# Performance work log

Measured on AMD Instinct MI355X. Metric: run time of the kernel, lower is better.

The kernel has to match this reference:

```python
import jax, jax.numpy as jnp
import numpy as np

B, S, E, H, L, NQ, FFN, V, C = 16, 2048, 256, 4, 2, 8, 512, 50257, 2
DK = E // H  # wires per attention head


def _pos_encoding(seq_len, dim):
    pos = jnp.arange(seq_len, dtype=jnp.float32)[:, None]
    div = jnp.exp(jnp.arange(0, dim, 2, dtype=jnp.float32) * (-np.log(10000.0) / dim))
    pe = jnp.zeros((seq_len, dim), dtype=jnp.float32)
    pe = pe.at[:, 0::2].set(jnp.sin(pos * div))
    pe = pe.at[:, 1::2].set(jnp.cos(pos * div))
    return pe


def _layernorm(x, g, b, eps=1e-5):
    m = x.mean(-1, keepdims=True)
    v = ((x - m) ** 2).mean(-1, keepdims=True)
    return (x - m) / jnp.sqrt(v + eps) * g + b


def setup_inputs() -> dict:
    key = jax.random.key(0)
    ks = jax.random.split(key, 9)
    f = lambda k, shape, s: jax.random.normal(k, shape, dtype=jnp.float32) * s
    return {
        "tokens": jax.random.randint(ks[0], (B, S), 0, V),
        "embed": f(ks[1], (V, E), 0.02),
        "attn_theta": f(ks[2], (L, DK), 1.0),
        "combine_w": f(ks[3], (L, E, E), 0.05),
        "combine_b": jnp.zeros((L, E), jnp.float32),
        "ffn_theta": f(ks[4], (L, NQ), 1.0),
        "lin1_w": f(ks[5], (L, NQ, FFN), 0.1),
        "lin1_b": jnp.zeros((L, FFN), jnp.float32),
        "lin2_w": f(ks[6], (L, FFN, E), 0.05),
        "lin2_b": jnp.zeros((L, E), jnp.float32),
        "ln1_g": jnp.ones((L, E), jnp.float32),
        "ln1_b": jnp.zeros((L, E), jnp.float32),
        "ln2_g": jnp.ones((L, E), jnp.float32),
        "ln2_b": jnp.zeros((L, E), jnp.float32),
        "cls_w": f(ks[7], (E, C), 0.05),
        "cls_b": jnp.zeros((C,), jnp.float32),
    }


def reference(tokens, embed, attn_theta, combine_w, combine_b, ffn_theta,
              lin1_w, lin1_b, lin2_w, lin2_b, ln1_g, ln1_b, ln2_g, ln2_b,
              cls_w, cls_b):
    # token embedding + sinusoidal positional encoding
    x = embed[tokens] + _pos_encoding(S, E)[None]  # [B,S,E]
    for l in range(L):
        # QuantumAttention: per-head RX-encode(x) then trainable RX(theta),
        # PauliZ expectation => cos(x + theta); same theta shared across heads,
        # head split/merge preserves feature layout => tile theta over heads.
        theta = jnp.tile(attn_theta[l], H)  # [E]
        attn = jnp.einsum('bse,ef->bsf', jnp.cos(x + theta), combine_w[l]) + combine_b[l]
        x = _layernorm(x + attn, ln1_g[l], ln1_b[l])
        # FeedForwardQuantum: RX-encode first NQ features, trainable RY(theta),
        # PauliZ expectation => cos(x) * cos(theta)
        q = jnp.cos(x[..., :NQ]) * jnp.cos(ffn_theta[l])  # [B,S,NQ]
        h = jax.nn.relu(jnp.einsum('bsn,nf->bsf', q, lin1_w[l]) + lin1_b[l])
        ffn = jnp.einsum('bsf,fe->bse', h, lin2_w[l]) + lin2_b[l]
        x = _layernorm(x + ffn, ln2_g[l], ln2_b[l])
    pooled = x.mean(axis=1)  # [B,E]
    return pooled @ cls_w + cls_b  # [B,C] logits
```

## Files before the change

### kernel.cpp

```cpp
#include <hip/hip_runtime.h>
#include <cstdint>
#include <cstddef>

#define SEQ   2048
#define EDIM  256
#define FFND  512
#define NBATCH 16
#define XLD   264

typedef unsigned short u16;
typedef __attribute__((ext_vector_type(8))) __bf16 bf16x8;
typedef __attribute__((ext_vector_type(4))) float f32x4;

__device__ __forceinline__ float bf2f(u16 u) {
  union { unsigned int w; float f; } v; v.w = ((unsigned int)u) << 16; return v.f;
}
__device__ __forceinline__ u16 f2bf(float f) {
  union { float f; unsigned int w; } v; v.f = f;
  unsigned int r = v.w + 0x7fffu + ((v.w >> 16) & 1u);
  return (u16)(r >> 16);
}
__device__ __forceinline__ float fast_cos(float x) {
  float r = x * 0.15915494309189535f;
  r = r - floorf(r);
  return __builtin_amdgcn_cosf(r);
}
__device__ __forceinline__ void unpack8(bf16x8 v, float* o) {
  const u16* p = (const u16*)&v;
  #pragma unroll
  for (int j = 0; j < 8; ++j) o[j] = bf2f(p[j]);
}

__global__ void sniff_kernel(const void* embed, int* flag) {
  int t = threadIdx.x;
  const u16* p = (const u16*)embed;
  int c = 0;
  #pragma unroll
  for (int j = 0; j < 8; ++j) {
    u16 v = p[t * 8 + j];
    int e = (v >> 7) & 0xff;
    c += (e > 128) ? 1 : 0;
  }
  #pragma unroll
  for (int d = 1; d < 64; d <<= 1) c += __shfl_xor(c, d);
  if (t == 0) *flag = (c > 64) ? 1 : 0;
}

struct CanonArgs { const void* p[14]; };

__global__ void canon_kernel(CanonArgs a, const int* __restrict__ flag, u16* __restrict__ dst) {
  const int off[15] = {0, 128, 131200, 131712, 131728, 139920, 140944, 403088,
                       403600, 404112, 404624, 405136, 405648, 406160, 406162};
  int i = blockIdx.x * 256 + threadIdx.x;
  if (i >= 406162) return;
  int isf32 = *flag;
  int s = 0;
  #pragma unroll
  for (int k = 0; k < 13; ++k) s += (i >= off[k + 1]) ? 1 : 0;
  int j = i - off[s];
  u16 v = isf32 ? f2bf(((const float*)a.p[s])[j]) : ((const u16*)a.p[s])[j];
  dst[i] = v;
}

__global__ void prep_kernel(const u16* __restrict__ cw, const u16* __restrict__ l2,
                            u16* __restrict__ cwT, u16* __restrict__ l2T) {
  int id = blockIdx.x * 256 + threadIdx.x;
  if (id < 2 * 256 * 256) {
    int l = id >> 16, rem = id & 65535;
    int kc = rem >> 11, n = (rem >> 3) & 255, kj = rem & 7;
    cwT[id] = cw[l * 65536 + (kc * 8 + kj) * 256 + n];
  } else {
    int j = id - 131072;
    if (j < 2 * 512 * 256) {
      int l = j >> 17, rem = j & 131071;
      int kc = rem >> 11, n = (rem >> 3) & 255, kj = rem & 7;
      l2T[j] = l2[l * 131072 + (kc * 8 + kj) * 256 + n];
    }
  }
}

__launch_bounds__(256, 2)
__global__ void mega_kernel(const int* __restrict__ tokens, const void* __restrict__ embed,
                            const int* __restrict__ flag, const u16* __restrict__ canon,
                            const u16* __restrict__ cwT, const u16* __restrict__ l2T,
                            float* __restrict__ pooled) {
  __shared__ u16 xt[64 * XLD];
  __shared__ union {
    struct { u16 Bt[256 * 64]; u16 At[64 * 64]; u16 qs[64 * 8]; } k;
    struct { float2 sstat[64][5]; float2 sms[64]; } ln;
  } sh;
  __shared__ u16 thL[64];

  const int tid = threadIdx.x;
  const int wave = tid >> 6, lane = tid & 63;
  const int fr = lane & 15, fq = lane >> 4;
  const int m0 = blockIdx.x * 64;
  const int isf32 = *flag;

  int cols[4];
  #pragma unroll
  for (int ni = 0; ni < 4; ++ni) cols[ni] = wave * 64 + ni * 16 + fr;

  {
    const float c0 = 9.210340371976184f / 128.f;
    const float inv2pi = 0.15915494309189535f;
    #pragma unroll
    for (int it = 0; it < 8; ++it) {
      int c = it * 256 + tid;
      int r = c >> 5, e8 = c & 31;
      int tok = tokens[m0 + r];
      float ev[8];
      if (isf32) {
        const float* ep = (const float*)embed + (size_t)tok * EDIM + e8 * 8;
        float4 a = *(const float4*)ep, b = *(const float4*)(ep + 4);
        ev[0]=a.x; ev[1]=a.y; ev[2]=a.z; ev[3]=a.w; ev[4]=b.x; ev[5]=b.y; ev[6]=b.z; ev[7]=b.w;
      } else {
        const u16* ep = (const u16*)embed + (size_t)tok * EDIM + e8 * 8;
        uint4 v = *(const uint4*)ep;
        unpack8(*(const bf16x8*)&v, ev);
      }
      int s = (m0 + r) & (SEQ - 1);
      u16 o[8];
      #pragma unroll
      for (int j = 0; j < 8; ++j) {
        int e = e8 * 8 + j, i = e >> 1;
        float rev = (float)s * (__expf(-(float)i * c0) * inv2pi);
        rev = rev - floorf(rev);
        float pe = (e & 1) ? __builtin_amdgcn_cosf(rev) : __builtin_amdgcn_sinf(rev);
        o[j] = f2bf(ev[j] + pe);
      }
      *(uint4*)(xt + r * XLD + e8 * 8) = *(const uint4*)o;
    }
  }
  __syncthreads();

  f32x4 acc[4][4];

  auto mfma_step = [&]() {
    const bf16x8* Av = (const bf16x8*)sh.k.At;
    const bf16x8* Bv = (const bf16x8*)sh.k.Bt;
    #pragma unroll
    for (int ks = 0; ks < 2; ++ks) {
      const int kc = ks * 4 + fq;
      bf16x8 af[4], bfv[4];
      #pragma unroll
      for (int mi = 0; mi < 4; ++mi) af[mi] = Av[kc * 64 + ((mi * 16 + fr) ^ kc)];
      #pragma unroll
      for (int ni = 0; ni < 4; ++ni) bfv[ni] = Bv[kc * 256 + cols[ni]];
      #pragma unroll
      for (int mi = 0; mi < 4; ++mi)
        #pragma unroll
        for (int ni = 0; ni < 4; ++ni)
          acc[mi][ni] = __builtin_amdgcn_mfma_f32_16x16x32_bf16(af[mi], bfv[ni], acc[mi][ni], 0, 0, 0);
    }
  };

  auto epilogue = [&](const u16* bias, const u16* gamma, const u16* beta) {
    float bcol[4];
    #pragma unroll
    for (int ni = 0; ni < 4; ++ni) bcol[ni] = bf2f(bias[cols[ni]]);
    #pragma unroll
    for (int mi = 0; mi < 4; ++mi)
      #pragma unroll
      for (int rg = 0; rg < 4; ++rg) {
        int lrow = mi * 16 + fq * 4 + rg;
        #pragma unroll
        for (int ni = 0; ni < 4; ++ni)
          acc[mi][ni][rg] += bf2f(xt[lrow * XLD + cols[ni]]) + bcol[ni];
      }
    float sr[4][4], sq[4][4];
    #pragma unroll
    for (int mi = 0; mi < 4; ++mi)
      #pragma unroll
      for (int rg = 0; rg < 4; ++rg) {
        float a = 0.f, b = 0.f;
        #pragma unroll
        for (int ni = 0; ni < 4; ++ni) { float t2 = acc[mi][ni][rg]; a += t2; b += t2 * t2; }
        sr[mi][rg] = a; sq[mi][rg] = b;
      }
    #pragma unroll
    for (int d = 1; d < 16; d <<= 1)
      #pragma unroll
      for (int mi = 0; mi < 4; ++mi)
        #pragma unroll
        for (int rg = 0; rg < 4; ++rg) {
          sr[mi][rg] += __shfl_xor(sr[mi][rg], d);
          sq[mi][rg] += __shfl_xor(sq[mi][rg], d);
        }
    if (fr == 0) {
      #pragma unroll
      for (int mi = 0; mi < 4; ++mi)
        #pragma unroll
        for (int rg = 0; rg < 4; ++rg)
          sh.ln.sstat[mi * 16 + fq * 4 + rg][wave] = float2{sr[mi][rg], sq[mi][rg]};
    }
    __syncthreads();
    if (tid < 64) {
      float s = 0.f, s2 = 0.f;
      #pragma unroll
      for (int w = 0; w < 4; ++w) { float2 p = sh.ln.sstat[tid][w]; s += p.x; s2 += p.y; }
      float mean = s * (1.f / 256.f);
      float var = fmaxf(s2 * (1.f / 256.f) - mean * mean, 0.f);
      sh.ln.sms[tid] = float2{mean, rsqrtf(var + 1e-5f)};
    }
    __syncthreads();
    float gcol[4], btc[4];
    #pragma unroll
    for (int ni = 0; ni < 4; ++ni) { gcol[ni] = bf2f(gamma[cols[ni]]); btc[ni] = bf2f(beta[cols[ni]]); }
    #pragma unroll
    for (int mi = 0; mi < 4; ++mi)
      #pragma unroll
      for (int rg = 0; rg < 4; ++rg) {
        int lrow = mi * 16 + fq * 4 + rg;
        float2 ms = sh.ln.sms[lrow];
        #pragma unroll
        for (int ni = 0; ni < 4; ++ni) {
          float o = (acc[mi][ni][rg] - ms.x) * ms.y * gcol[ni] + btc[ni];
          xt[lrow * XLD + cols[ni]] = f2bf(o);
        }
      }
    __syncthreads();
  };

  for (int l = 0; l < 2; ++l) {
    if (tid < 8) ((uint4*)thL)[tid] = ((const uint4*)(canon + l * 64))[tid];
    __syncthreads();
    #pragma unroll
    for (int i = 0; i < 4; ++i)
      #pragma unroll
      for (int j = 0; j < 4; ++j) acc[i][j] = {0.f, 0.f, 0.f, 0.f};
    {
      const u16* Bbase = cwT + l * 65536;
      for (int k0 = 0; k0 < 256; k0 += 64) {
        const u16* bsrc = Bbase + (k0 >> 3) * 2048;
        #pragma unroll
        for (int it = 0; it < 8; ++it) {
          int c = tid + it * 256;
          __builtin_amdgcn_global_load_lds(
              (const __attribute__((address_space(1))) void*)(bsrc + (size_t)c * 8),
              (__attribute__((address_space(3))) void*)(sh.k.Bt + c * 8), 16, 0, 0);
        }
        #pragma unroll
        for (int it = 0; it < 2; ++it) {
          int c = it * 256 + tid;
          int f8 = c >> 6, r = c & 63;
          uint4 g = *(const uint4*)(xt + r * XLD + k0 + f8 * 8);
          u16* gp = (u16*)&g;
          #pragma unroll
          for (int j = 0; j < 8; ++j)
            gp[j] = f2bf(fast_cos(bf2f(gp[j]) + bf2f(thL[f8 * 8 + j])));
          ((uint4*)sh.k.At)[f8 * 64 + (r ^ f8)] = g;
        }
        __syncthreads();
        mfma_step();
        __syncthreads();
      }
    }
    epilogue(canon + 131200 + l * 256, canon + 403600 + l * 256, canon + 404112 + l * 256);

    #pragma unroll
    for (int rep = 0; rep < 2; ++rep) {
      int idx = tid + rep * 256;
      int r = idx >> 3, n = idx & 7;
      float cth = fast_cos(bf2f(canon[131712 + l * 8 + n]));
      sh.k.qs[r * 8 + n] = f2bf(fast_cos(bf2f(xt[r * XLD + n])) * cth);
    }
    __syncthreads();

    #pragma unroll
    for (int i = 0; i < 4; ++i)
      #pragma unroll
      for (int j = 0; j < 4; ++j) acc[i][j] = {0.f, 0.f, 0.f, 0.f};
    {
      const u16* B2 = l2T + l * 131072;
      const u16* w1 = canon + 131728 + l * 4096;
      const u16* b1 = canon + 139920 + l * 512;
      for (int k0 = 0; k0 < 512; k0 += 64) {
        const u16* bsrc = B2 + (k0 >> 3) * 2048;
        #pragma unroll
        for (int it = 0; it < 8; ++it) {
          int c = tid + it * 256;
          __builtin_amdgcn_global_load_lds(
              (const __attribute__((address_space(1))) void*)(bsrc + (size_t)c * 8),
              (__attribute__((address_space(3))) void*)(sh.k.Bt + c * 8), 16, 0, 0);
        }
        #pragma unroll
        for (int it = 0; it < 2; ++it) {
          int c = it * 256 + tid;
          int kc = c >> 6, r = c & 63;
          int cc = (k0 >> 3) + kc;
          float qf[8], hv[8];
          unpack8(((const bf16x8*)sh.k.qs)[r], qf);
          { uint4 bv = *(const uint4*)(b1 + cc * 8); unpack8(*(const bf16x8*)&bv, hv); }
          #pragma unroll
          for (int n = 0; n < 8; ++n) {
            uint4 wv = *(const uint4*)(w1 + n * 512 + cc * 8);
            float wf[8];
            unpack8(*(const bf16x8*)&wv, wf);
            #pragma unroll
            for (int j = 0; j < 8; ++j) hv[j] += qf[n] * wf[j];
          }
          uint4 g; u16* gp = (u16*)&g;
          #pragma unroll
          for (int j = 0; j < 8; ++j) gp[j] = f2bf(fmaxf(hv[j], 0.f));
          ((uint4*)sh.k.At)[kc * 64 + (r ^ kc)] = g;
        }
        __syncthreads();
        mfma_step();
        __syncthreads();
      }
    }
    epilogue(canon + 403088 + l * 256, canon + 404624 + l * 256, canon + 405136 + l * 256);
  }

  {
    float s = 0.f;
    #pragma unroll 8
    for (int r = 0; r < 64; ++r) s += bf2f(xt[r * XLD + tid]);
    atomicAdd(&pooled[(m0 >> 11) * EDIM + tid], s);
  }
}

__global__ void logits_kernel(const float* __restrict__ pooled, const u16* __restrict__ clsw,
                              const u16* __restrict__ clsb, const int* __restrict__ flag,
                              void* __restrict__ out) {
  int t = threadIdx.x;
  int b = t >> 4, sub = t & 15;
  float a0 = 0.f, a1 = 0.f;
  #pragma unroll
  for (int j = 0; j < 16; ++j) {
    int e = sub * 16 + j;
    float p = pooled[b * 256 + e];
    a0 += p * bf2f(clsw[e * 2 + 0]);
    a1 += p * bf2f(clsw[e * 2 + 1]);
  }
  #pragma unroll
  for (int d = 1; d < 16; d <<= 1) {
    a0 += __shfl_xor(a0, d);
    a1 += __shfl_xor(a1, d);
  }
  if (sub == 0) {
    float o0 = a0 * (1.f / 2048.f) + bf2f(clsb[0]);
    float o1 = a1 * (1.f / 2048.f) + bf2f(clsb[1]);
    if (*flag) {
      ((float*)out)[b * 2 + 0] = o0; ((float*)out)[b * 2 + 1] = o1;
    } else {
      ((u16*)out)[b * 2 + 0] = f2bf(o0); ((u16*)out)[b * 2 + 1] = f2bf(o1);
    }
  }
}

extern "C" void kernel_launch(void* const* d_in, const int* in_sizes, int n_in,
                              void* d_out, int out_size, void* d_ws, size_t ws_size,
                              hipStream_t stream) {
  const int* tokens = (const int*)d_in[0];

  char* ws = (char*)d_ws;
  u16*   canon  = (u16*)(ws + 0);
  u16*   cwT    = (u16*)(ws + 1048576);
  u16*   l2T    = (u16*)(ws + 1310720);
  float* pooled = (float*)(ws + 1835008);
  int*   flag   = (int*)(ws + 1851392);

  sniff_kernel<<<1, 64, 0, stream>>>(d_in[1], flag);

  CanonArgs ca;
  for (int i = 0; i < 14; ++i) ca.p[i] = d_in[i + 2];
  canon_kernel<<<1587, 256, 0, stream>>>(ca, flag, canon);

  prep_kernel<<<1536, 256, 0, stream>>>(canon + 128, canon + 140944, cwT, l2T);

  hipMemsetAsync(pooled, 0, NBATCH * EDIM * sizeof(float), stream);

  mega_kernel<<<512, 256, 0, stream>>>(tokens, d_in[1], flag, canon, cwT, l2T, pooled);

  logits_kernel<<<1, 256, 0, stream>>>(pooled, canon + 405648, canon + 406160, flag, d_out);
}
```

Measured before the change: 217.9 us.

## Move FFN lin1 to MFMA, precompute PE divisors, shrink canon copy

The scalar FMA computation of the FFN first layer (q @ lin1_w + b, ReLU) is replaced with MFMA instructions. Weights are held in registers and results are written straight into the swizzled A tile, and the first lin2 B tile is prefetched earlier. Positional-encoding divisors are computed once into a small table, so the per-element exp disappears. Biases are folded into the accumulator init, and packed bf16 conversion uses v_cvt_pk_bf16_f32. The canon/prep kernels now convert the large weights directly from the inputs, so the full copy of combine_w and lin2_w is no longer made twice. The zero-padded MFMA for the K=8 product wastes most lanes, and the inline asm conversion changes rounding details slightly.

```diff
diff --git a/kernel.cpp b/kernel.cpp
--- a/kernel.cpp
+++ b/kernel.cpp
@@ -4,7 +4,6 @@
 
 #define SEQ   2048
 #define EDIM  256
-#define FFND  512
 #define NBATCH 16
 #define XLD   264
 
@@ -20,6 +19,11 @@
   unsigned int r = v.w + 0x7fffu + ((v.w >> 16) & 1u);
   return (u16)(r >> 16);
 }
+__device__ __forceinline__ unsigned int pk2(float lo, float hi) {
+  unsigned int d;
+  asm("v_cvt_pk_bf16_f32 %0, %1, %2" : "=v"(d) : "v"(lo), "v"(hi));
+  return d;
+}
 __device__ __forceinline__ float fast_cos(float x) {
   float r = x * 0.15915494309189535f;
   r = r - floorf(r);
@@ -46,35 +50,50 @@
   if (t == 0) *flag = (c > 64) ? 1 : 0;
 }
 
-struct CanonArgs { const void* p[14]; };
-
-__global__ void canon_kernel(CanonArgs a, const int* __restrict__ flag, u16* __restrict__ dst) {
-  const int off[15] = {0, 128, 131200, 131712, 131728, 139920, 140944, 403088,
-                       403600, 404112, 404624, 405136, 405648, 406160, 406162};
+struct CanonArgs { const void* p[11]; };
+
+__global__ void canon_kernel(CanonArgs a, const int* __restrict__ flag,
+                             u16* __restrict__ dst, float* __restrict__ divt) {
+  const int off[12] = {0, 128, 640, 656, 1680, 2192, 2704, 3216, 3728, 4240, 4752, 4754};
   int i = blockIdx.x * 256 + threadIdx.x;
-  if (i >= 406162) return;
+  if (i < 128) {
+    const float c0 = 9.210340371976184f / 128.f;
+    const float inv2pi = 0.15915494309189535f;
+    divt[i] = __expf(-(float)i * c0) * inv2pi;
+  }
+  if (i >= 4754) return;
   int isf32 = *flag;
   int s = 0;
   #pragma unroll
-  for (int k = 0; k < 13; ++k) s += (i >= off[k + 1]) ? 1 : 0;
+  for (int k = 0; k < 10; ++k) s += (i >= off[k + 1]) ? 1 : 0;
   int j = i - off[s];
-  u16 v = isf32 ? f2bf(((const float*)a.p[s])[j]) : ((const u16*)a.p[s])[j];
-  dst[i] = v;
-}
-
-__global__ void prep_kernel(const u16* __restrict__ cw, const u16* __restrict__ l2,
-                            u16* __restrict__ cwT, u16* __restrict__ l2T) {
+  dst[i] = isf32 ? f2bf(((const float*)a.p[s])[j]) : ((const u16*)a.p[s])[j];
+}
+
+__global__ void prep_kernel(const void* __restrict__ cw, const void* __restrict__ w1,
+                            const void* __restrict__ l2, const int* __restrict__ flag,
+                            u16* __restrict__ cwT, u16* __restrict__ l2T,
+                            u16* __restrict__ w1T) {
   int id = blockIdx.x * 256 + threadIdx.x;
-  if (id < 2 * 256 * 256) {
+  int isf32 = *flag;
+  if (id < 131072) {
     int l = id >> 16, rem = id & 65535;
     int kc = rem >> 11, n = (rem >> 3) & 255, kj = rem & 7;
-    cwT[id] = cw[l * 65536 + (kc * 8 + kj) * 256 + n];
+    int idx = l * 65536 + (kc * 8 + kj) * 256 + n;
+    cwT[id] = isf32 ? f2bf(((const float*)cw)[idx]) : ((const u16*)cw)[idx];
+  } else if (id < 131072 + 262144) {
+    int j = id - 131072;
+    int l = j >> 17, rem = j & 131071;
+    int kc = rem >> 11, n = (rem >> 3) & 255, kj = rem & 7;
+    int idx = l * 131072 + (kc * 8 + kj) * 256 + n;
+    l2T[j] = isf32 ? f2bf(((const float*)l2)[idx]) : ((const u16*)l2)[idx];
   } else {
-    int j = id - 131072;
-    if (j < 2 * 512 * 256) {
-      int l = j >> 17, rem = j & 131071;
-      int kc = rem >> 11, n = (rem >> 3) & 255, kj = rem & 7;
-      l2T[j] = l2[l * 131072 + (kc * 8 + kj) * 256 + n];
+    int j = id - (131072 + 262144);
+    if (j < 2 * 512 * 8) {
+      int l = j >> 12, rem = j & 4095;
+      int c = rem >> 3, jj = rem & 7;
+      int idx = l * 4096 + jj * 512 + c;
+      w1T[j] = isf32 ? f2bf(((const float*)w1)[idx]) : ((const u16*)w1)[idx];
     }
   }
 }
@@ -83,6 +102,7 @@
 __global__ void mega_kernel(const int* __restrict__ tokens, const void* __restrict__ embed,
                             const int* __restrict__ flag, const u16* __restrict__ canon,
                             const u16* __restrict__ cwT, const u16* __restrict__ l2T,
+                            const u16* __restrict__ w1T, const float* __restrict__ divt,
                             float* __restrict__ pooled) {
   __shared__ u16 xt[64 * XLD];
   __shared__ union {
@@ -102,8 +122,6 @@
   for (int ni = 0; ni < 4; ++ni) cols[ni] = wave * 64 + ni * 16 + fr;
 
   {
-    const float c0 = 9.210340371976184f / 128.f;
-    const float inv2pi = 0.15915494309189535f;
     #pragma unroll
     for (int it = 0; it < 8; ++it) {
       int c = it * 256 + tid;
@@ -119,17 +137,18 @@
         uint4 v = *(const uint4*)ep;
         unpack8(*(const bf16x8*)&v, ev);
       }
-      int s = (m0 + r) & (SEQ - 1);
-      u16 o[8];
-      #pragma unroll
-      for (int j = 0; j < 8; ++j) {
-        int e = e8 * 8 + j, i = e >> 1;
-        float rev = (float)s * (__expf(-(float)i * c0) * inv2pi);
-        rev = rev - floorf(rev);
-        float pe = (e & 1) ? __builtin_amdgcn_cosf(rev) : __builtin_amdgcn_sinf(rev);
-        o[j] = f2bf(ev[j] + pe);
-      }
-      *(uint4*)(xt + r * XLD + e8 * 8) = *(const uint4*)o;
+      float sf = (float)((m0 + r) & (SEQ - 1));
+      float4 dv = *(const float4*)(divt + e8 * 4);
+      float r0 = sf * dv.x; r0 -= floorf(r0);
+      float r1 = sf * dv.y; r1 -= floorf(r1);
+      float r2 = sf * dv.z; r2 -= floorf(r2);
+      float r3 = sf * dv.w; r3 -= floorf(r3);
+      uint4 o;
+      o.x = pk2(ev[0] + __builtin_amdgcn_sinf(r0), ev[1] + __builtin_amdgcn_cosf(r0));
+      o.y = pk2(ev[2] + __builtin_amdgcn_sinf(r1), ev[3] + __builtin_amdgcn_cosf(r1));
+      o.z = pk2(ev[4] + __builtin_amdgcn_sinf(r2), ev[5] + __builtin_amdgcn_cosf(r2));
+      o.w = pk2(ev[6] + __builtin_amdgcn_sinf(r3), ev[7] + __builtin_amdgcn_cosf(r3));
+      *(uint4*)(xt + r * XLD + e8 * 8) = o;
     }
   }
   __syncthreads();
@@ -155,10 +174,16 @@
     }
   };
 
-  auto epilogue = [&](const u16* bias, const u16* gamma, const u16* beta) {
-    float bcol[4];
-    #pragma unroll
-    for (int ni = 0; ni < 4; ++ni) bcol[ni] = bf2f(bias[cols[ni]]);
+  auto acc_init = [&](const u16* bias) {
+    #pragma unroll
+    for (int ni = 0; ni < 4; ++ni) {
+      float b = bf2f(bias[cols[ni]]);
+      #pragma unroll
+      for (int mi = 0; mi < 4; ++mi) acc[mi][ni] = {b, b, b, b};
+    }
+  };
+
+  auto epilogue = [&](const u16* gamma, const u16* beta) {
     #pragma unroll
     for (int mi = 0; mi < 4; ++mi)
       #pragma unroll
@@ -166,7 +191,7 @@
         int lrow = mi * 16 + fq * 4 + rg;
         #pragma unroll
         for (int ni = 0; ni < 4; ++ni)
-          acc[mi][ni][rg] += bf2f(xt[lrow * XLD + cols[ni]]) + bcol[ni];
+          acc[mi][ni][rg] += bf2f(xt[lrow * XLD + cols[ni]]);
       }
     float sr[4][4], sq[4][4];
     #pragma unroll
@@ -225,10 +250,7 @@
   for (int l = 0; l < 2; ++l) {
     if (tid < 8) ((uint4*)thL)[tid] = ((const uint4*)(canon + l * 64))[tid];
     __syncthreads();
-    #pragma unroll
-    for (int i = 0; i < 4; ++i)
-      #pragma unroll
-      for (int j = 0; j < 4; ++j) acc[i][j] = {0.f, 0.f, 0.f, 0.f};
+    acc_init(canon + 128 + l * 256);
     {
       const u16* Bbase = cwT + l * 65536;
       for (int k0 = 0; k0 < 256; k0 += 64) {
@@ -245,38 +267,79 @@
           int c = it * 256 + tid;
           int f8 = c >> 6, r = c & 63;
           uint4 g = *(const uint4*)(xt + r * XLD + k0 + f8 * 8);
-          u16* gp = (u16*)&g;
+          const u16* gp = (const u16*)&g;
+          float cv[8];
           #pragma unroll
           for (int j = 0; j < 8; ++j)
-            gp[j] = f2bf(fast_cos(bf2f(gp[j]) + bf2f(thL[f8 * 8 + j])));
-          ((uint4*)sh.k.At)[f8 * 64 + (r ^ f8)] = g;
+            cv[j] = fast_cos(bf2f(gp[j]) + bf2f(thL[f8 * 8 + j]));
+          uint4 o;
+          o.x = pk2(cv[0], cv[1]); o.y = pk2(cv[2], cv[3]);
+          o.z = pk2(cv[4], cv[5]); o.w = pk2(cv[6], cv[7]);
+          ((uint4*)sh.k.At)[f8 * 64 + (r ^ f8)] = o;
         }
         __syncthreads();
         mfma_step();
         __syncthreads();
       }
     }
-    epilogue(canon + 131200 + l * 256, canon + 403600 + l * 256, canon + 404112 + l * 256);
-
+    epilogue(canon + 2192 + l * 256, canon + 2704 + l * 256);
+
+    const u16* B2 = l2T + (size_t)l * 131072;
+    #pragma unroll
+    for (int it = 0; it < 8; ++it) {
+      int c = tid + it * 256;
+      __builtin_amdgcn_global_load_lds(
+          (const __attribute__((address_space(1))) void*)(B2 + (size_t)c * 8),
+          (__attribute__((address_space(3))) void*)(sh.k.Bt + c * 8), 16, 0, 0);
+    }
     #pragma unroll
     for (int rep = 0; rep < 2; ++rep) {
       int idx = tid + rep * 256;
       int r = idx >> 3, n = idx & 7;
-      float cth = fast_cos(bf2f(canon[131712 + l * 8 + n]));
+      float cth = fast_cos(bf2f(canon[640 + l * 8 + n]));
       sh.k.qs[r * 8 + n] = f2bf(fast_cos(bf2f(xt[r * XLD + n])) * cth);
     }
+    bf16x8 aW1[8]; uint2 b1p[8];
+    #pragma unroll
+    for (int c = 0; c < 8; ++c) {
+      uint4 t = {0u, 0u, 0u, 0u};
+      if (fq == 0) t = *(const uint4*)(w1T + (size_t)l * 4096 + (size_t)(c * 64 + wave * 16 + fr) * 8);
+      aW1[c] = *(const bf16x8*)&t;
+      b1p[c] = *(const uint2*)(canon + 656 + l * 512 + c * 64 + wave * 16 + fq * 4);
+    }
     __syncthreads();
-
-    #pragma unroll
-    for (int i = 0; i < 4; ++i)
-      #pragma unroll
-      for (int j = 0; j < 4; ++j) acc[i][j] = {0.f, 0.f, 0.f, 0.f};
-    {
-      const u16* B2 = l2T + l * 131072;
-      const u16* w1 = canon + 131728 + l * 4096;
-      const u16* b1 = canon + 139920 + l * 512;
-      for (int k0 = 0; k0 < 512; k0 += 64) {
-        const u16* bsrc = B2 + (k0 >> 3) * 2048;
+    bf16x8 bq[4];
+    #pragma unroll
+    for (int ni = 0; ni < 4; ++ni) {
+      uint4 t = {0u, 0u, 0u, 0u};
+      if (fq == 0) t = ((const uint4*)sh.k.qs)[ni * 16 + fr];
+      bq[ni] = *(const bf16x8*)&t;
+    }
+    acc_init(canon + 1680 + l * 256);
+    #pragma unroll
+    for (int c8 = 0; c8 < 8; ++c8) {
+      {
+        float b0 = bf2f((u16)(b1p[c8].x & 0xffffu)), b1v = bf2f((u16)(b1p[c8].x >> 16));
+        float b2 = bf2f((u16)(b1p[c8].y & 0xffffu)), b3 = bf2f((u16)(b1p[c8].y >> 16));
+        const int kcL = wave * 2 + (fq >> 1);
+        const int halfoff = (fq & 1) * 4;
+        #pragma unroll
+        for (int ni = 0; ni < 4; ++ni) {
+          f32x4 hacc;
+          hacc[0] = b0; hacc[1] = b1v; hacc[2] = b2; hacc[3] = b3;
+          hacc = __builtin_amdgcn_mfma_f32_16x16x32_bf16(aW1[c8], bq[ni], hacc, 0, 0, 0);
+          float h0 = fmaxf(hacc[0], 0.f), h1 = fmaxf(hacc[1], 0.f);
+          float h2 = fmaxf(hacc[2], 0.f), h3 = fmaxf(hacc[3], 0.f);
+          uint2 dw; dw.x = pk2(h0, h1); dw.y = pk2(h2, h3);
+          int r = ni * 16 + fr;
+          *(uint2*)(sh.k.At + ((kcL * 64 + (r ^ kcL)) * 8 + halfoff)) = dw;
+        }
+      }
+      __syncthreads();
+      mfma_step();
+      __syncthreads();
+      if (c8 < 7) {
+        const u16* bsrc = B2 + (size_t)(c8 + 1) * 16384;
         #pragma unroll
         for (int it = 0; it < 8; ++it) {
           int c = tid + it * 256;
@@ -284,33 +347,9 @@
               (const __attribute__((address_space(1))) void*)(bsrc + (size_t)c * 8),
               (__attribute__((address_space(3))) void*)(sh.k.Bt + c * 8), 16, 0, 0);
         }
-        #pragma unroll
-        for (int it = 0; it < 2; ++it) {
-          int c = it * 256 + tid;
-          int kc = c >> 6, r = c & 63;
-          int cc = (k0 >> 3) + kc;
-          float qf[8], hv[8];
-          unpack8(((const bf16x8*)sh.k.qs)[r], qf);
-          { uint4 bv = *(const uint4*)(b1 + cc * 8); unpack8(*(const bf16x8*)&bv, hv); }
-          #pragma unroll
-          for (int n = 0; n < 8; ++n) {
-            uint4 wv = *(const uint4*)(w1 + n * 512 + cc * 8);
-            float wf[8];
-            unpack8(*(const bf16x8*)&wv, wf);
-            #pragma unroll
-            for (int j = 0; j < 8; ++j) hv[j] += qf[n] * wf[j];
-          }
-          uint4 g; u16* gp = (u16*)&g;
-          #pragma unroll
-          for (int j = 0; j < 8; ++j) gp[j] = f2bf(fmaxf(hv[j], 0.f));
-          ((uint4*)sh.k.At)[kc * 64 + (r ^ kc)] = g;
-        }
-        __syncthreads();
-        mfma_step();
-        __syncthreads();
-      }
-    }
-    epilogue(canon + 403088 + l * 256, canon + 404624 + l * 256, canon + 405136 + l * 256);
+      }
+    }
+    epilogue(canon + 3216 + l * 256, canon + 3728 + l * 256);
   }
 
   {
@@ -357,22 +396,26 @@
 
   char* ws = (char*)d_ws;
   u16*   canon  = (u16*)(ws + 0);
-  u16*   cwT    = (u16*)(ws + 1048576);
-  u16*   l2T    = (u16*)(ws + 1310720);
-  float* pooled = (float*)(ws + 1835008);
-  int*   flag   = (int*)(ws + 1851392);
+  u16*   cwT    = (u16*)(ws + 16384);
+  u16*   l2T    = (u16*)(ws + 278528);
+  u16*   w1T    = (u16*)(ws + 802816);
+  float* pooled = (float*)(ws + 819200);
+  int*   flag   = (int*)(ws + 835584);
+  float* divt   = (float*)(ws + 835600);
 
   sniff_kernel<<<1, 64, 0, stream>>>(d_in[1], flag);
 
   CanonArgs ca;
-  for (int i = 0; i < 14; ++i) ca.p[i] = d_in[i + 2];
-  canon_kernel<<<1587, 256, 0, stream>>>(ca, flag, canon);
-
-  prep_kernel<<<1536, 256, 0, stream>>>(canon + 128, canon + 140944, cwT, l2T);
+  ca.p[0] = d_in[2];  ca.p[1] = d_in[4];  ca.p[2] = d_in[5];  ca.p[3] = d_in[7];
+  ca.p[4] = d_in[9];  ca.p[5] = d_in[10]; ca.p[6] = d_in[11]; ca.p[7] = d_in[12];
+  ca.p[8] = d_in[13]; ca.p[9] = d_in[14]; ca.p[10] = d_in[15];
+  canon_kernel<<<19, 256, 0, stream>>>(ca, flag, canon, divt);
+
+  prep_kernel<<<1568, 256, 0, stream>>>(d_in[3], d_in[6], d_in[8], flag, cwT, l2T, w1T);
 
   hipMemsetAsync(pooled, 0, NBATCH * EDIM * sizeof(float), stream);
 
-  mega_kernel<<<512, 256, 0, stream>>>(tokens, d_in[1], flag, canon, cwT, l2T, pooled);
-
-  logits_kernel<<<1, 256, 0, stream>>>(pooled, canon + 405648, canon + 406160, flag, d_out);
-}
+  mega_kernel<<<512, 256, 0, stream>>>(tokens, d_in[1], flag, canon, cwT, l2T, w1T, divt, pooled);
+
+  logits_kernel<<<1, 256, 0, stream>>>(pooled, canon + 4240, canon + 4752, flag, d_out);
+}
```

Result: faster. 180.5 us (-17.1%).
